# Kernel optimization log

Hardware: AMD Instinct MI355X
Metric: run time of the kernel (lower is better)

Reference implementation:

```python
import jax, jax.numpy as jnp
import numpy as np
from jax.ops import segment_sum, segment_max

N_NODES = 10000
N_EDGES = 160000
N_GRAPHS = 32
IN_DIM = 128
HID = 256
HEADS = 4


def setup_inputs() -> dict:
    key = jax.random.key(0)
    ks = jax.random.split(key, 12)
    x = jax.random.normal(ks[0], (N_NODES, IN_DIM), dtype=jnp.float32)
    edge_index = jax.random.randint(ks[1], (2, N_EDGES), 0, N_NODES, dtype=jnp.int64)
    batch = jnp.sort(jax.random.randint(ks[2], (N_NODES,), 0, N_GRAPHS, dtype=jnp.int64))
    s = 0.05
    params = {
        "W1": jax.random.normal(ks[3], (IN_DIM, HID), dtype=jnp.float32) * s,
        "b1": jnp.zeros((HID,), dtype=jnp.float32),
        "W2": jax.random.normal(ks[4], (HID, HID), dtype=jnp.float32) * s,
        "b2": jnp.zeros((HID,), dtype=jnp.float32),
        "Wg": jax.random.normal(ks[5], (HID, HEADS * HID), dtype=jnp.float32) * s,
        "att_src": jax.random.normal(ks[6], (HEADS, HID), dtype=jnp.float32) * s,
        "att_dst": jax.random.normal(ks[7], (HEADS, HID), dtype=jnp.float32) * s,
        "bg": jnp.zeros((HID,), dtype=jnp.float32),
        "W_heads": jax.random.normal(ks[8], (HID, 4), dtype=jnp.float32) * s,
        "b_heads": jnp.zeros((4,), dtype=jnp.float32),
    }
    return {"x": x, "edge_index": edge_index, "batch": batch, **params}


def _add_self_loops(edge_index, n):
    loop = jnp.arange(n, dtype=edge_index.dtype)
    src = jnp.concatenate([edge_index[0], loop])
    dst = jnp.concatenate([edge_index[1], loop])
    return src, dst


def _gcn_conv(x, W, b, src, dst, n):
    # PyG GCNConv: add self-loops, symmetric normalization D^-1/2 A D^-1/2
    h = x @ W                                   # [N, out]
    deg = segment_sum(jnp.ones_like(src, dtype=h.dtype), dst, num_segments=n)
    dinv = jax.lax.rsqrt(jnp.maximum(deg, 1e-12))
    coef = dinv[src] * dinv[dst]                # [E+N]
    out = segment_sum(h[src] * coef[:, None], dst, num_segments=n)
    return out + b


def _gat_conv(x, Wg, att_src, att_dst, bg, src, dst, n):
    # PyG GATConv(heads=4, concat=False): mean over heads, leaky_relu slope 0.2
    h = (x @ Wg).reshape(n, HEADS, HID)         # [N, H, C]
    a_src = jnp.einsum('nhc,hc->nh', h, att_src)
    a_dst = jnp.einsum('nhc,hc->nh', h, att_dst)
    e = jax.nn.leaky_relu(a_src[src] + a_dst[dst], 0.2)   # [E+N, H]
    m = segment_max(e, dst, num_segments=n)
    e = jnp.exp(e - m[dst])
    z = segment_sum(e, dst, num_segments=n)
    alpha = e / (z[dst] + 1e-16)                # softmax over edges into each dst
    out = segment_sum(h[src] * alpha[:, :, None], dst, num_segments=n)  # [N, H, C]
    return out.mean(axis=1) + bg


def reference(x, edge_index, batch, W1, b1, W2, b2, Wg, att_src, att_dst, bg, W_heads, b_heads):
    n = x.shape[0]
    src, dst = _add_self_loops(edge_index, n)
    h1 = jax.nn.relu(_gcn_conv(x, W1, b1, src, dst, n))
    h2 = jax.nn.relu(_gcn_conv(h1, W2, b2, src, dst, n))
    h3 = jax.nn.relu(_gat_conv(h2, Wg, att_src, att_dst, bg, src, dst, n))
    # global_mean_pool
    ones = jnp.ones((n,), dtype=h3.dtype)
    cnt = segment_sum(ones, batch, num_segments=N_GRAPHS)
    pooled = segment_sum(h3, batch, num_segments=N_GRAPHS) / jnp.maximum(cnt, 1.0)[:, None]
    # four scalar heads stacked: cols = [energy_absorption, elastic_modulus, ballistic_limit, penetration_resistance]
    return pooled @ W_heads + b_heads           # [G, 4]
```

## Files before the change

### kernel.cpp

```cpp
#include <hip/hip_runtime.h>
#include <cmath>

#define IN_DIM 128
#define HID 256
#define NHEADS 4
#define NGRAPHS 32

typedef unsigned short u16;
typedef __attribute__((ext_vector_type(8))) short bfrag8;
typedef __attribute__((ext_vector_type(4))) float f32x4;

__device__ __forceinline__ u16 f2bf(float x) {
  unsigned u = __float_as_uint(x);
  unsigned r = (u + 0x7fffu + ((u >> 16) & 1u)) >> 16;
  return (u16)r;
}
__device__ __forceinline__ float bf2f(u16 v) {
  return __uint_as_float(((unsigned)v) << 16);
}
__device__ __forceinline__ float lof(unsigned u) { return __uint_as_float(u << 16); }
__device__ __forceinline__ float hif(unsigned u) { return __uint_as_float(u & 0xffff0000u); }
__device__ __forceinline__ float lrelu02(float x) { return x > 0.f ? x : 0.2f * x; }

#define GACC(U, W)                                                   \
  acc[0] += (W) * lof((U).x); acc[1] += (W) * hif((U).x);            \
  acc[2] += (W) * lof((U).y); acc[3] += (W) * hif((U).y);            \
  acc[4] += (W) * lof((U).z); acc[5] += (W) * hif((U).z);            \
  acc[6] += (W) * lof((U).w); acc[7] += (W) * hif((U).w);

#define GACC2(U, W)                                                  \
  a0 += (W) * lof((U).x); a1 += (W) * hif((U).x);                    \
  a2 += (W) * lof((U).y); a3 += (W) * hif((U).y);

__global__ __launch_bounds__(256) void count_edges_k(const int* __restrict__ dst,
                                                     int* __restrict__ cnt, int E) {
  int i = blockIdx.x * 256 + threadIdx.x;
  if (i < E) atomicAdd(&cnt[dst[i]], 1);
}

__global__ __launch_bounds__(256) void fill_csr_k(const int* __restrict__ src,
                                                  const int* __restrict__ dst,
                                                  const int* __restrict__ row_ptr,
                                                  int* __restrict__ cursor,
                                                  int* __restrict__ csr_src, int E) {
  int i = blockIdx.x * 256 + threadIdx.x;
  if (i < E) {
    int d = dst[i];
    int p = atomicAdd(&cursor[d], 1);
    csr_src[row_ptr[d] + p] = src[i];
  }
}

__device__ void scan_dev(const int* __restrict__ cnt, int* __restrict__ row_ptr,
                         float* __restrict__ dinv, int n) {
  __shared__ int s_w[4];
  __shared__ int s_off[4];
  __shared__ int s_tot;
  int tid = threadIdx.x, wv = tid >> 6, lane = tid & 63;
  int carry = 0;
  int nch = (n + 255) >> 8;
  for (int c = 0; c < nch; c++) {
    int i = (c << 8) + tid;
    int v = (i < n) ? cnt[i] : 0;
    int incl = v;
    #pragma unroll
    for (int off = 1; off < 64; off <<= 1) {
      int t = __shfl_up(incl, off);
      if (lane >= off) incl += t;
    }
    if (lane == 63) s_w[wv] = incl;
    __syncthreads();
    if (tid == 0) {
      int a0 = s_w[0], a1 = s_w[1], a2 = s_w[2], a3 = s_w[3];
      s_off[0] = 0; s_off[1] = a0; s_off[2] = a0 + a1; s_off[3] = a0 + a1 + a2;
      s_tot = a0 + a1 + a2 + a3;
    }
    __syncthreads();
    int excl = incl - v + s_off[wv] + carry;
    if (i < n) {
      row_ptr[i] = excl;
      dinv[i] = rsqrtf((float)(v + 1));
    }
    carry += s_tot;
    __syncthreads();
  }
  if (tid == 0) row_ptr[n] = carry;
}

__device__ void pack_a_dev(const float* __restrict__ A, u16* __restrict__ Ap,
                           int K, int KT, int wid, int lane) {
  int fm = wid / KT, kt = wid - fm * KT;
  int m = fm * 16 + (lane & 15);
  int kb = kt * 32 + (lane >> 4) * 8;
  const float* src = A + (size_t)m * K + kb;
  float4 v0 = *(const float4*)src;
  float4 v1 = *(const float4*)(src + 4);
  float vv[8] = {v0.x, v0.y, v0.z, v0.w, v1.x, v1.y, v1.z, v1.w};
  u16 hi[8], lo[8];
  #pragma unroll
  for (int j = 0; j < 8; j++) {
    u16 h = f2bf(vv[j]);
    hi[j] = h;
    lo[j] = f2bf(vv[j] - bf2f(h));
  }
  u16* dstp = Ap + ((size_t)fm * KT + kt) * 1024 + lane * 8;
  *(ushort4*)(dstp)       = make_ushort4(hi[0], hi[1], hi[2], hi[3]);
  *(ushort4*)(dstp + 4)   = make_ushort4(hi[4], hi[5], hi[6], hi[7]);
  *(ushort4*)(dstp + 512) = make_ushort4(lo[0], lo[1], lo[2], lo[3]);
  *(ushort4*)(dstp + 516) = make_ushort4(lo[4], lo[5], lo[6], lo[7]);
}

__device__ void pack_b_dev(const float* __restrict__ B, u16* __restrict__ Bp,
                           int N, int KT, int wid, int lane) {
  int fn = wid / KT, kt = wid - fn * KT;
  int n = fn * 16 + (lane & 15);
  int kb = kt * 32 + (lane >> 4) * 8;
  float vv[8];
  #pragma unroll
  for (int j = 0; j < 8; j++) vv[j] = B[(size_t)(kb + j) * N + n];
  u16 hi[8], lo[8];
  #pragma unroll
  for (int j = 0; j < 8; j++) {
    u16 h = f2bf(vv[j]);
    hi[j] = h;
    lo[j] = f2bf(vv[j] - bf2f(h));
  }
  u16* dstp = Bp + ((size_t)fn * KT + kt) * 1024 + lane * 8;
  *(ushort4*)(dstp)       = make_ushort4(hi[0], hi[1], hi[2], hi[3]);
  *(ushort4*)(dstp + 4)   = make_ushort4(hi[4], hi[5], hi[6], hi[7]);
  *(ushort4*)(dstp + 512) = make_ushort4(lo[0], lo[1], lo[2], lo[3]);
  *(ushort4*)(dstp + 516) = make_ushort4(lo[4], lo[5], lo[6], lo[7]);
}

__global__ __launch_bounds__(256) void prep_k(const float* __restrict__ x,
                                              const float* __restrict__ W1,
                                              const float* __restrict__ W2,
                                              const float* __restrict__ Wg,
                                              const float* __restrict__ att_src,
                                              const float* __restrict__ att_dst,
                                              const int* __restrict__ cnt,
                                              int* __restrict__ row_ptr,
                                              float* __restrict__ dinv,
                                              u16* __restrict__ xp,
                                              u16* __restrict__ w1p,
                                              u16* __restrict__ w2p,
                                              u16* __restrict__ wgp,
                                              float* __restrict__ w_s,
                                              float* __restrict__ w_d,
                                              int NFM, int N) {
  __shared__ float red_s[4][NHEADS];
  __shared__ float red_d[4][NHEADS];
  int b = blockIdx.x;
  int tid = threadIdx.x;
  int lane = tid & 63;
  if (b == 0) {
    scan_dev(cnt, row_ptr, dinv, N);
    return;
  }
  b -= 1;
  int XB = NFM;
  if (b < XB) {
    int wid = b * 4 + (tid >> 6);
    if (wid < NFM * 4) pack_a_dev(x, xp, IN_DIM, 4, wid, lane);
  } else if (b < XB + 16) {
    pack_b_dev(W1, w1p, HID, 4, (b - XB) * 4 + (tid >> 6), lane);
  } else if (b < XB + 48) {
    pack_b_dev(W2, w2p, HID, 8, (b - XB - 16) * 4 + (tid >> 6), lane);
  } else if (b < XB + 176) {
    pack_b_dev(Wg, wgp, NHEADS * HID, 8, (b - XB - 48) * 4 + (tid >> 6), lane);
  } else {
    int k = b - (XB + 176);
    int c = tid, wvv = c >> 6, ln = c & 63;
    #pragma unroll
    for (int h = 0; h < NHEADS; h++) {
      float w = Wg[(size_t)k * (NHEADS * HID) + h * HID + c];
      float vs = w * att_src[h * HID + c];
      float vd = w * att_dst[h * HID + c];
      #pragma unroll
      for (int off = 32; off; off >>= 1) {
        vs += __shfl_xor(vs, off);
        vd += __shfl_xor(vd, off);
      }
      if (ln == 0) { red_s[wvv][h] = vs; red_d[wvv][h] = vd; }
    }
    __syncthreads();
    if (c < NHEADS)
      w_s[k * NHEADS + c] = red_s[0][c] + red_s[1][c] + red_s[2][c] + red_s[3][c];
    else if (c < 2 * NHEADS) {
      int h = c - NHEADS;
      w_d[k * NHEADS + h] = red_d[0][h] + red_d[1][h] + red_d[2][h] + red_d[3][h];
    }
  }
}

template <int KT, int LDC, bool ALO>
__global__ __launch_bounds__(256) void mfma_gemm_k(const u16* __restrict__ Ap,
                                                   const u16* __restrict__ Bp,
                                                   u16* __restrict__ Cb, int M) {
  int tid = threadIdx.x;
  int w = tid >> 6, lane = tid & 63;
  int wm = w >> 1, wn = w & 1;
  int fm0 = blockIdx.y * 4 + wm * 2;
  int fn0 = blockIdx.x * 4 + wn * 2;
  f32x4 acc[2][2] = {};
  #pragma unroll
  for (int kt = 0; kt < KT; kt++) {
    bfrag8 a_hi[2], a_lo[2], b_hi[2], b_lo[2];
    #pragma unroll
    for (int f = 0; f < 2; f++) {
      const u16* pa = Ap + ((size_t)(fm0 + f) * KT + kt) * 1024 + lane * 8;
      a_hi[f] = *(const bfrag8*)pa;
      if constexpr (ALO) a_lo[f] = *(const bfrag8*)(pa + 512);
      const u16* pb = Bp + ((size_t)(fn0 + f) * KT + kt) * 1024 + lane * 8;
      b_hi[f] = *(const bfrag8*)pb;
      b_lo[f] = *(const bfrag8*)(pb + 512);
    }
    #pragma unroll
    for (int f = 0; f < 2; f++) {
      #pragma unroll
      for (int g = 0; g < 2; g++) {
        acc[f][g] = __builtin_amdgcn_mfma_f32_16x16x32_bf16(a_hi[f], b_hi[g], acc[f][g], 0, 0, 0);
        acc[f][g] = __builtin_amdgcn_mfma_f32_16x16x32_bf16(a_hi[f], b_lo[g], acc[f][g], 0, 0, 0);
        if constexpr (ALO)
          acc[f][g] = __builtin_amdgcn_mfma_f32_16x16x32_bf16(a_lo[f], b_hi[g], acc[f][g], 0, 0, 0);
      }
    }
  }
  int r0 = (lane >> 4) * 4;
  int cl = lane & 15;
  #pragma unroll
  for (int f = 0; f < 2; f++) {
    #pragma unroll
    for (int g = 0; g < 2; g++) {
      int col = (fn0 + g) * 16 + cl;
      #pragma unroll
      for (int r = 0; r < 4; r++) {
        int row = (fm0 + f) * 16 + r0 + r;
        if (row < M) Cb[(size_t)row * LDC + col] = f2bf(acc[f][g][r]);
      }
    }
  }
}

template <bool LOGITS, bool PACK_LO>
__global__ __launch_bounds__(256) void gcn_agg_k(const u16* __restrict__ t,
                                                 const int* __restrict__ row_ptr,
                                                 const int* __restrict__ csr_src,
                                                 const float* __restrict__ dinv,
                                                 const float* __restrict__ bias,
                                                 u16* __restrict__ apack,
                                                 const float* __restrict__ w_s,
                                                 const float* __restrict__ w_d,
                                                 float4* __restrict__ a_src4,
                                                 float4* __restrict__ a_dst4, int N) {
  int wv = threadIdx.x >> 6, lane = threadIdx.x & 63;
  int i = blockIdx.x * 4 + wv;
  if (i >= N) return;
  float di = dinv[i];
  int c4 = lane * 4;
  int beg = row_ptr[i], end = row_ptr[i + 1];
  float a0, a1, a2, a3;
  {
    uint2 u = *(const uint2*)&t[(size_t)i * HID + c4];
    float w = di * di;
    a0 = w * lof(u.x); a1 = w * hif(u.x); a2 = w * lof(u.y); a3 = w * hif(u.y);
  }
  int e = beg;
  for (; e + 3 < end; e += 4) {
    int s0 = csr_src[e + 0], s1 = csr_src[e + 1];
    int s2 = csr_src[e + 2], s3 = csr_src[e + 3];
    float w0 = dinv[s0] * di, w1 = dinv[s1] * di;
    float w2 = dinv[s2] * di, w3 = dinv[s3] * di;
    uint2 u0 = *(const uint2*)&t[(size_t)s0 * HID + c4];
    uint2 u1 = *(const uint2*)&t[(size_t)s1 * HID + c4];
    uint2 u2 = *(const uint2*)&t[(size_t)s2 * HID + c4];
    uint2 u3 = *(const uint2*)&t[(size_t)s3 * HID + c4];
    GACC2(u0, w0); GACC2(u1, w1); GACC2(u2, w2); GACC2(u3, w3);
  }
  for (; e < end; e++) {
    int s = csr_src[e];
    float w = dinv[s] * di;
    uint2 u = *(const uint2*)&t[(size_t)s * HID + c4];
    GACC2(u, w);
  }
  float4 bv = *(const float4*)&bias[c4];
  float v0 = fmaxf(a0 + bv.x, 0.f), v1 = fmaxf(a1 + bv.y, 0.f);
  float v2 = fmaxf(a2 + bv.z, 0.f), v3 = fmaxf(a3 + bv.w, 0.f);
  {
    int fm = i >> 4, kt = c4 >> 5;
    int pl = (i & 15) + 16 * ((c4 >> 3) & 3);
    int j = c4 & 7;
    size_t base = ((size_t)fm * 8 + kt) * 1024 + pl * 8 + j;
    u16 h0 = f2bf(v0), h1 = f2bf(v1), h2 = f2bf(v2), h3 = f2bf(v3);
    *(ushort4*)&apack[base] = make_ushort4(h0, h1, h2, h3);
    if constexpr (PACK_LO)
      *(ushort4*)&apack[base + 512] =
          make_ushort4(f2bf(v0 - bf2f(h0)), f2bf(v1 - bf2f(h1)),
                       f2bf(v2 - bf2f(h2)), f2bf(v3 - bf2f(h3)));
  }
  if constexpr (LOGITS) {
    const float4* ws4 = (const float4*)w_s;
    const float4* wd4 = (const float4*)w_d;
    float4 s0 = ws4[c4 + 0], s1 = ws4[c4 + 1], s2 = ws4[c4 + 2], s3 = ws4[c4 + 3];
    float4 d0 = wd4[c4 + 0], d1 = wd4[c4 + 1], d2 = wd4[c4 + 2], d3 = wd4[c4 + 3];
    float ps0 = v0 * s0.x + v1 * s1.x + v2 * s2.x + v3 * s3.x;
    float ps1 = v0 * s0.y + v1 * s1.y + v2 * s2.y + v3 * s3.y;
    float ps2 = v0 * s0.z + v1 * s1.z + v2 * s2.z + v3 * s3.z;
    float ps3 = v0 * s0.w + v1 * s1.w + v2 * s2.w + v3 * s3.w;
    float pd0 = v0 * d0.x + v1 * d1.x + v2 * d2.x + v3 * d3.x;
    float pd1 = v0 * d0.y + v1 * d1.y + v2 * d2.y + v3 * d3.y;
    float pd2 = v0 * d0.z + v1 * d1.z + v2 * d2.z + v3 * d3.z;
    float pd3 = v0 * d0.w + v1 * d1.w + v2 * d2.w + v3 * d3.w;
    #pragma unroll
    for (int off = 32; off; off >>= 1) {
      ps0 += __shfl_xor(ps0, off); ps1 += __shfl_xor(ps1, off);
      ps2 += __shfl_xor(ps2, off); ps3 += __shfl_xor(ps3, off);
      pd0 += __shfl_xor(pd0, off); pd1 += __shfl_xor(pd1, off);
      pd2 += __shfl_xor(pd2, off); pd3 += __shfl_xor(pd3, off);
    }
    if (lane == 0) {
      a_src4[i] = make_float4(ps0, ps1, ps2, ps3);
      a_dst4[i] = make_float4(pd0, pd1, pd2, pd3);
    }
  }
}

__global__ __launch_bounds__(256) void gat_agg_k(const u16* __restrict__ hgT,
                                                 const int* __restrict__ row_ptr,
                                                 const int* __restrict__ csr_src,
                                                 const float4* __restrict__ a_src4,
                                                 const float4* __restrict__ a_dst4,
                                                 const float* __restrict__ bg,
                                                 float* __restrict__ out, int N) {
  __shared__ int s_src[4][64];
  __shared__ float s_al[4][2][64];
  __shared__ float s_comb[2][32][9];
  int wv = threadIdx.x >> 6, lane = threadIdx.x & 63;
  int nodeSlot = wv >> 1, half = wv & 1;
  int i = blockIdx.x * 2 + nodeSlot;
  if (i >= N) { __syncthreads(); return; }
  int beg = row_ptr[i], end = row_ptr[i + 1];
  int deg = end - beg;
  float4 ad = a_dst4[i];
  int hsel = lane >> 5;
  const u16* rowbase = hgT + half * 512 + lane * 8;
  float acc[8];
  #pragma unroll
  for (int j = 0; j < 8; j++) acc[j] = 0.f;

  if (deg <= 63) {
    int s = (lane < deg) ? csr_src[beg + lane] : i;
    bool valid = (lane <= deg);
    float4 as = a_src4[s];
    float l0 = valid ? lrelu02(as.x + ad.x) : -INFINITY;
    float l1 = valid ? lrelu02(as.y + ad.y) : -INFINITY;
    float l2 = valid ? lrelu02(as.z + ad.z) : -INFINITY;
    float l3 = valid ? lrelu02(as.w + ad.w) : -INFINITY;
    float m0 = l0, m1 = l1, m2 = l2, m3 = l3;
    #pragma unroll
    for (int off = 32; off; off >>= 1) {
      m0 = fmaxf(m0, __shfl_xor(m0, off)); m1 = fmaxf(m1, __shfl_xor(m1, off));
      m2 = fmaxf(m2, __shfl_xor(m2, off)); m3 = fmaxf(m3, __shfl_xor(m3, off));
    }
    float e0 = valid ? expf(l0 - m0) : 0.f;
    float e1 = valid ? expf(l1 - m1) : 0.f;
    float e2 = valid ? expf(l2 - m2) : 0.f;
    float e3 = valid ? expf(l3 - m3) : 0.f;
    float z0 = e0, z1 = e1, z2 = e2, z3 = e3;
    #pragma unroll
    for (int off = 32; off; off >>= 1) {
      z0 += __shfl_xor(z0, off); z1 += __shfl_xor(z1, off);
      z2 += __shfl_xor(z2, off); z3 += __shfl_xor(z3, off);
    }
    s_src[wv][lane] = s;
    if (half == 0) {
      s_al[wv][0][lane] = e0 / (z0 + 1e-16f);
      s_al[wv][1][lane] = e1 / (z1 + 1e-16f);
    } else {
      s_al[wv][0][lane] = e2 / (z2 + 1e-16f);
      s_al[wv][1][lane] = e3 / (z3 + 1e-16f);
    }
    int nk = deg + 1;
    int e = 0;
    for (; e + 3 < nk; e += 4) {
      int sa = s_src[wv][e + 0], sb = s_src[wv][e + 1];
      int sc = s_src[wv][e + 2], sd = s_src[wv][e + 3];
      float wa = s_al[wv][hsel][e + 0], wb = s_al[wv][hsel][e + 1];
      float wc = s_al[wv][hsel][e + 2], wd = s_al[wv][hsel][e + 3];
      uint4 ua = *(const uint4*)(rowbase + (size_t)sa * 1024);
      uint4 ub = *(const uint4*)(rowbase + (size_t)sb * 1024);
      uint4 uc = *(const uint4*)(rowbase + (size_t)sc * 1024);
      uint4 ud = *(const uint4*)(rowbase + (size_t)sd * 1024);
      GACC(ua, wa); GACC(ub, wb); GACC(uc, wc); GACC(ud, wd);
    }
    for (; e < nk; e++) {
      int sa = s_src[wv][e];
      float wa = s_al[wv][hsel][e];
      uint4 ua = *(const uint4*)(rowbase + (size_t)sa * 1024);
      GACC(ua, wa);
    }
  } else {
    float4 asi = a_src4[i];
    float ls0 = lrelu02(asi.x + ad.x), ls1 = lrelu02(asi.y + ad.y);
    float ls2 = lrelu02(asi.z + ad.z), ls3 = lrelu02(asi.w + ad.w);
    float m0 = ls0, m1 = ls1, m2 = ls2, m3 = ls3;
    for (int e = beg + lane; e < end; e += 64) {
      float4 as = a_src4[csr_src[e]];
      m0 = fmaxf(m0, lrelu02(as.x + ad.x)); m1 = fmaxf(m1, lrelu02(as.y + ad.y));
      m2 = fmaxf(m2, lrelu02(as.z + ad.z)); m3 = fmaxf(m3, lrelu02(as.w + ad.w));
    }
    #pragma unroll
    for (int off = 32; off; off >>= 1) {
      m0 = fmaxf(m0, __shfl_xor(m0, off)); m1 = fmaxf(m1, __shfl_xor(m1, off));
      m2 = fmaxf(m2, __shfl_xor(m2, off)); m3 = fmaxf(m3, __shfl_xor(m3, off));
    }
    float z0 = (lane == 0) ? expf(ls0 - m0) : 0.f;
    float z1 = (lane == 0) ? expf(ls1 - m1) : 0.f;
    float z2 = (lane == 0) ? expf(ls2 - m2) : 0.f;
    float z3 = (lane == 0) ? expf(ls3 - m3) : 0.f;
    for (int e = beg + lane; e < end; e += 64) {
      float4 as = a_src4[csr_src[e]];
      z0 += expf(lrelu02(as.x + ad.x) - m0); z1 += expf(lrelu02(as.y + ad.y) - m1);
      z2 += expf(lrelu02(as.z + ad.z) - m2); z3 += expf(lrelu02(as.w + ad.w) - m3);
    }
    #pragma unroll
    for (int off = 32; off; off >>= 1) {
      z0 += __shfl_xor(z0, off); z1 += __shfl_xor(z1, off);
      z2 += __shfl_xor(z2, off); z3 += __shfl_xor(z3, off);
    }
    float iz0 = 1.f / (z0 + 1e-16f), iz1 = 1.f / (z1 + 1e-16f);
    float iz2 = 1.f / (z2 + 1e-16f), iz3 = 1.f / (z3 + 1e-16f);
    {
      float w0 = expf(ls0 - m0) * iz0, w1 = expf(ls1 - m1) * iz1;
      float w2 = expf(ls2 - m2) * iz2, w3 = expf(ls3 - m3) * iz3;
      float aw = (half == 0) ? (hsel == 0 ? w0 : w1) : (hsel == 0 ? w2 : w3);
      uint4 u = *(const uint4*)(rowbase + (size_t)i * 1024);
      GACC(u, aw);
    }
    for (int base = beg; base < end; base += 64) {
      int mc = min(64, end - base);
      if (lane < mc) {
        int s = csr_src[base + lane];
        float4 as = a_src4[s];
        s_src[wv][lane] = s;
        if (half == 0) {
          s_al[wv][0][lane] = expf(lrelu02(as.x + ad.x) - m0) * iz0;
          s_al[wv][1][lane] = expf(lrelu02(as.y + ad.y) - m1) * iz1;
        } else {
          s_al[wv][0][lane] = expf(lrelu02(as.z + ad.z) - m2) * iz2;
          s_al[wv][1][lane] = expf(lrelu02(as.w + ad.w) - m3) * iz3;
        }
      }
      for (int e = 0; e < mc; e++) {
        int sa = s_src[wv][e];
        float wa = s_al[wv][hsel][e];
        uint4 ua = *(const uint4*)(rowbase + (size_t)sa * 1024);
        GACC(ua, wa);
      }
    }
  }
  #pragma unroll
  for (int j = 0; j < 8; j++) acc[j] += __shfl_xor(acc[j], 32);
  if (half == 1 && lane < 32) {
    #pragma unroll
    for (int j = 0; j < 8; j++) s_comb[nodeSlot][lane][j] = acc[j];
  }
  __syncthreads();
  if (half == 0 && lane < 32) {
    int cb = lane * 8;
    float o[8];
    #pragma unroll
    for (int j = 0; j < 8; j++)
      o[j] = fmaxf((acc[j] + s_comb[nodeSlot][lane][j]) * 0.25f + bg[cb + j], 0.f);
    float* op = out + (size_t)i * HID + cb;
    *(float4*)(op + 0) = make_float4(o[0], o[1], o[2], o[3]);
    *(float4*)(op + 4) = make_float4(o[4], o[5], o[6], o[7]);
  }
}

__global__ __launch_bounds__(256) void pool_head_k(const float* __restrict__ h3,
                                                   const int* __restrict__ batch,
                                                   const float* __restrict__ W_heads,
                                                   const float* __restrict__ b_heads,
                                                   float* __restrict__ out, int N) {
  int g = blockIdx.x >> 3;
  int part = blockIdx.x & 7;
  int c = threadIdx.x;
  __shared__ int s_bounds[2];
  if (c < 2) {
    int target = g + c;
    int lo = 0, hi = N;
    while (lo < hi) {
      int mid = (lo + hi) >> 1;
      if (batch[mid] < target) lo = mid + 1; else hi = mid;
    }
    s_bounds[c] = lo;
  }
  __syncthreads();
  int i0 = s_bounds[0], i1 = s_bounds[1];
  float acc0 = 0.f, acc1 = 0.f;
  int i = i0 + part;
  for (; i + 8 < i1; i += 16) {
    acc0 += h3[(size_t)i * HID + c];
    acc1 += h3[(size_t)(i + 8) * HID + c];
  }
  if (i < i1) acc0 += h3[(size_t)i * HID + c];
  float acc = acc0 + acc1;
  float invc = 1.f / fmaxf((float)(i1 - i0), 1.f);
  float4 wh = *(const float4*)&W_heads[c * 4];
  float p0 = acc * wh.x, p1 = acc * wh.y, p2 = acc * wh.z, p3 = acc * wh.w;
  int lane = c & 63, wv = c >> 6;
  #pragma unroll
  for (int off = 32; off; off >>= 1) {
    p0 += __shfl_xor(p0, off); p1 += __shfl_xor(p1, off);
    p2 += __shfl_xor(p2, off); p3 += __shfl_xor(p3, off);
  }
  __shared__ float s_red[4][4];
  if (lane == 0) { s_red[wv][0] = p0; s_red[wv][1] = p1; s_red[wv][2] = p2; s_red[wv][3] = p3; }
  __syncthreads();
  if (c < 4) {
    float r = s_red[0][c] + s_red[1][c] + s_red[2][c] + s_red[3][c];
    atomicAdd(&out[g * 4 + c], r * invc + b_heads[c] * 0.125f);
  }
}

extern "C" void kernel_launch(void* const* d_in, const int* in_sizes, int n_in,
                              void* d_out, int out_size, void* d_ws, size_t ws_size,
                              hipStream_t stream) {
  const float* x = (const float*)d_in[0];
  const int* ei = (const int*)d_in[1];
  const int* batch = (const int*)d_in[2];
  const float* W1 = (const float*)d_in[3];
  const float* b1 = (const float*)d_in[4];
  const float* W2 = (const float*)d_in[5];
  const float* b2 = (const float*)d_in[6];
  const float* Wg = (const float*)d_in[7];
  const float* att_src = (const float*)d_in[8];
  const float* att_dst = (const float*)d_in[9];
  const float* bg = (const float*)d_in[10];
  const float* W_heads = (const float*)d_in[11];
  const float* b_heads = (const float*)d_in[12];
  float* out = (float*)d_out;

  const int N = in_sizes[0] / IN_DIM;
  const int E = in_sizes[1] / 2;
  const int* src = ei;
  const int* dst = ei + E;

  const int NFM = N / 16;
  const int NFMP = ((N + 63) / 64) * 4;

  char* ws = (char*)d_ws;
  size_t off = 0;
  auto take = [&](size_t bytes) -> char* {
    char* p = ws + off;
    off = (off + bytes + 255) & ~(size_t)255;
    return p;
  };
  int* cnt      = (int*)take((size_t)N * 4);
  int* cursor   = (int*)take((size_t)N * 4);
  size_t zero_span = off;
  int* row_ptr  = (int*)take((size_t)(N + 1) * 4);
  int* csr_src  = (int*)take((size_t)E * 4);
  float* dinv   = (float*)take((size_t)N * 4);
  float4* a_src4 = (float4*)take((size_t)N * 16);
  float4* a_dst4 = (float4*)take((size_t)N * 16);
  float* w_s    = (float*)take((size_t)HID * NHEADS * 4);
  float* w_d    = (float*)take((size_t)HID * NHEADS * 4);
  u16*   tb     = (u16*)take((size_t)N * HID * 2);
  float* h3     = (float*)take((size_t)N * HID * 4);
  u16*   hgT    = (u16*)take((size_t)N * NHEADS * HID * 2);
  u16*   xp     = (u16*)take((size_t)NFMP * 4 * 1024 * 2);
  u16*   h1p    = (u16*)take((size_t)NFMP * 8 * 1024 * 2);
  u16*   h2p    = (u16*)take((size_t)NFMP * 8 * 1024 * 2);
  u16*   w1p    = (u16*)take((size_t)16 * 4 * 1024 * 2);
  u16*   w2p    = (u16*)take((size_t)16 * 8 * 1024 * 2);
  u16*   wgp    = (u16*)take((size_t)64 * 8 * 1024 * 2);

  hipMemsetAsync(cnt, 0, zero_span, stream);
  hipMemsetAsync(out, 0, (size_t)out_size * 4, stream);

  int eb = (E + 255) / 256;
  count_edges_k<<<eb, 256, 0, stream>>>(dst, cnt, E);
  prep_k<<<1 + NFM + 176 + 256, 256, 0, stream>>>(x, W1, W2, Wg, att_src, att_dst,
                                                  cnt, row_ptr, dinv,
                                                  xp, w1p, w2p, wgp, w_s, w_d, NFM, N);
  fill_csr_k<<<eb, 256, 0, stream>>>(src, dst, row_ptr, cursor, csr_src, E);

  int mg64 = (N + 63) / 64;
  int ng4 = (N + 3) / 4;
  int ng2 = (N + 1) / 2;
  mfma_gemm_k<4, HID, true><<<dim3(4, mg64), 256, 0, stream>>>(xp, w1p, tb, N);
  gcn_agg_k<false, true><<<ng4, 256, 0, stream>>>(tb, row_ptr, csr_src, dinv, b1,
                                                  h1p, nullptr, nullptr, nullptr, nullptr, N);
  mfma_gemm_k<8, HID, true><<<dim3(4, mg64), 256, 0, stream>>>(h1p, w2p, tb, N);
  gcn_agg_k<true, false><<<ng4, 256, 0, stream>>>(tb, row_ptr, csr_src, dinv, b2,
                                                  h2p, w_s, w_d, a_src4, a_dst4, N);
  mfma_gemm_k<8, NHEADS * HID, false><<<dim3(16, mg64), 256, 0, stream>>>(h2p, wgp, hgT, N);
  gat_agg_k<<<ng2, 256, 0, stream>>>(hgT, row_ptr, csr_src, a_src4, a_dst4, bg, h3, N);
  pool_head_k<<<NGRAPHS * 8, 256, 0, stream>>>(h3, batch, W_heads, b_heads, out, N);
}
```

Measured before the change: 197.9 us.

## Fuse mean-pool and regression heads into GAT aggregation; drop A-lo split precision

The global mean pool and the four-column head projection move into the GAT aggregation epilogue. Each node projects its ReLU output onto W_heads, scales by a precomputed inverse graph count, and atomically adds into the output. The output is initialised with the bias in prep_k, which also computes the per-graph counts by binary search. This removes the h3 write and read and the separate pool kernel. Separately, the low-order bf16 part of the A operand is no longer packed or multiplied, which cuts one MFMA in three for the first two GEMMs at some cost in accuracy. The trade-off is many more atomics per graph output and float atomic nondeterminism.

```diff
diff --git a/kernel.cpp b/kernel.cpp
--- a/kernel.cpp
+++ b/kernel.cpp
@@ -87,6 +87,7 @@
   if (tid == 0) row_ptr[n] = carry;
 }
 
+template <bool LO>
 __device__ void pack_a_dev(const float* __restrict__ A, u16* __restrict__ Ap,
                            int K, int KT, int wid, int lane) {
   int fm = wid / KT, kt = wid - fm * KT;
@@ -96,18 +97,19 @@
   float4 v0 = *(const float4*)src;
   float4 v1 = *(const float4*)(src + 4);
   float vv[8] = {v0.x, v0.y, v0.z, v0.w, v1.x, v1.y, v1.z, v1.w};
-  u16 hi[8], lo[8];
-  #pragma unroll
-  for (int j = 0; j < 8; j++) {
-    u16 h = f2bf(vv[j]);
-    hi[j] = h;
-    lo[j] = f2bf(vv[j] - bf2f(h));
-  }
+  u16 hi[8];
+  #pragma unroll
+  for (int j = 0; j < 8; j++) hi[j] = f2bf(vv[j]);
   u16* dstp = Ap + ((size_t)fm * KT + kt) * 1024 + lane * 8;
-  *(ushort4*)(dstp)       = make_ushort4(hi[0], hi[1], hi[2], hi[3]);
-  *(ushort4*)(dstp + 4)   = make_ushort4(hi[4], hi[5], hi[6], hi[7]);
-  *(ushort4*)(dstp + 512) = make_ushort4(lo[0], lo[1], lo[2], lo[3]);
-  *(ushort4*)(dstp + 516) = make_ushort4(lo[4], lo[5], lo[6], lo[7]);
+  *(ushort4*)(dstp)     = make_ushort4(hi[0], hi[1], hi[2], hi[3]);
+  *(ushort4*)(dstp + 4) = make_ushort4(hi[4], hi[5], hi[6], hi[7]);
+  if constexpr (LO) {
+    u16 lo[8];
+    #pragma unroll
+    for (int j = 0; j < 8; j++) lo[j] = f2bf(vv[j] - bf2f(hi[j]));
+    *(ushort4*)(dstp + 512) = make_ushort4(lo[0], lo[1], lo[2], lo[3]);
+    *(ushort4*)(dstp + 516) = make_ushort4(lo[4], lo[5], lo[6], lo[7]);
+  }
 }
 
 __device__ void pack_b_dev(const float* __restrict__ B, u16* __restrict__ Bp,
@@ -147,6 +149,10 @@
                                               u16* __restrict__ wgp,
                                               float* __restrict__ w_s,
                                               float* __restrict__ w_d,
+                                              const int* __restrict__ batch,
+                                              float* __restrict__ ginv,
+                                              const float* __restrict__ b_heads,
+                                              float* __restrict__ outp,
                                               int NFM, int N) {
   __shared__ float red_s[4][NHEADS];
   __shared__ float red_d[4][NHEADS];
@@ -161,14 +167,14 @@
   int XB = NFM;
   if (b < XB) {
     int wid = b * 4 + (tid >> 6);
-    if (wid < NFM * 4) pack_a_dev(x, xp, IN_DIM, 4, wid, lane);
+    if (wid < NFM * 4) pack_a_dev<false>(x, xp, IN_DIM, 4, wid, lane);
   } else if (b < XB + 16) {
     pack_b_dev(W1, w1p, HID, 4, (b - XB) * 4 + (tid >> 6), lane);
   } else if (b < XB + 48) {
     pack_b_dev(W2, w2p, HID, 8, (b - XB - 16) * 4 + (tid >> 6), lane);
   } else if (b < XB + 176) {
     pack_b_dev(Wg, wgp, NHEADS * HID, 8, (b - XB - 48) * 4 + (tid >> 6), lane);
-  } else {
+  } else if (b < XB + 432) {
     int k = b - (XB + 176);
     int c = tid, wvv = c >> 6, ln = c & 63;
     #pragma unroll
@@ -190,10 +196,25 @@
       int h = c - NHEADS;
       w_d[k * NHEADS + h] = red_d[0][h] + red_d[1][h] + red_d[2][h] + red_d[3][h];
     }
-  }
-}
-
-template <int KT, int LDC, bool ALO>
+  } else {
+    __shared__ int s_b[NGRAPHS + 1];
+    if (tid <= NGRAPHS) {
+      int target = tid;
+      int lo = 0, hi = N;
+      while (lo < hi) {
+        int mid = (lo + hi) >> 1;
+        if (batch[mid] < target) lo = mid + 1; else hi = mid;
+      }
+      s_b[tid] = lo;
+    }
+    __syncthreads();
+    if (tid < NGRAPHS)
+      ginv[tid] = 1.f / fmaxf((float)(s_b[tid + 1] - s_b[tid]), 1.f);
+    if (tid < NGRAPHS * 4) outp[tid] = b_heads[tid & 3];
+  }
+}
+
+template <int KT, int LDC>
 __global__ __launch_bounds__(256) void mfma_gemm_k(const u16* __restrict__ Ap,
                                                    const u16* __restrict__ Bp,
                                                    u16* __restrict__ Cb, int M) {
@@ -205,12 +226,11 @@
   f32x4 acc[2][2] = {};
   #pragma unroll
   for (int kt = 0; kt < KT; kt++) {
-    bfrag8 a_hi[2], a_lo[2], b_hi[2], b_lo[2];
+    bfrag8 a_hi[2], b_hi[2], b_lo[2];
     #pragma unroll
     for (int f = 0; f < 2; f++) {
       const u16* pa = Ap + ((size_t)(fm0 + f) * KT + kt) * 1024 + lane * 8;
       a_hi[f] = *(const bfrag8*)pa;
-      if constexpr (ALO) a_lo[f] = *(const bfrag8*)(pa + 512);
       const u16* pb = Bp + ((size_t)(fn0 + f) * KT + kt) * 1024 + lane * 8;
       b_hi[f] = *(const bfrag8*)pb;
       b_lo[f] = *(const bfrag8*)(pb + 512);
@@ -221,8 +241,6 @@
       for (int g = 0; g < 2; g++) {
         acc[f][g] = __builtin_amdgcn_mfma_f32_16x16x32_bf16(a_hi[f], b_hi[g], acc[f][g], 0, 0, 0);
         acc[f][g] = __builtin_amdgcn_mfma_f32_16x16x32_bf16(a_hi[f], b_lo[g], acc[f][g], 0, 0, 0);
-        if constexpr (ALO)
-          acc[f][g] = __builtin_amdgcn_mfma_f32_16x16x32_bf16(a_lo[f], b_hi[g], acc[f][g], 0, 0, 0);
       }
     }
   }
@@ -242,7 +260,7 @@
   }
 }
 
-template <bool LOGITS, bool PACK_LO>
+template <bool LOGITS>
 __global__ __launch_bounds__(256) void gcn_agg_k(const u16* __restrict__ t,
                                                  const int* __restrict__ row_ptr,
                                                  const int* __restrict__ csr_src,
@@ -291,12 +309,7 @@
     int pl = (i & 15) + 16 * ((c4 >> 3) & 3);
     int j = c4 & 7;
     size_t base = ((size_t)fm * 8 + kt) * 1024 + pl * 8 + j;
-    u16 h0 = f2bf(v0), h1 = f2bf(v1), h2 = f2bf(v2), h3 = f2bf(v3);
-    *(ushort4*)&apack[base] = make_ushort4(h0, h1, h2, h3);
-    if constexpr (PACK_LO)
-      *(ushort4*)&apack[base + 512] =
-          make_ushort4(f2bf(v0 - bf2f(h0)), f2bf(v1 - bf2f(h1)),
-                       f2bf(v2 - bf2f(h2)), f2bf(v3 - bf2f(h3)));
+    *(ushort4*)&apack[base] = make_ushort4(f2bf(v0), f2bf(v1), f2bf(v2), f2bf(v3));
   }
   if constexpr (LOGITS) {
     const float4* ws4 = (const float4*)w_s;
@@ -331,7 +344,10 @@
                                                  const float4* __restrict__ a_src4,
                                                  const float4* __restrict__ a_dst4,
                                                  const float* __restrict__ bg,
-                                                 float* __restrict__ out, int N) {
+                                                 const float* __restrict__ W_heads,
+                                                 const float* __restrict__ ginv,
+                                                 const int* __restrict__ batch,
+                                                 float* __restrict__ outp, int N) {
   __shared__ int s_src[4][64];
   __shared__ float s_al[4][2][64];
   __shared__ float s_comb[2][32][9];
@@ -468,59 +484,26 @@
   __syncthreads();
   if (half == 0 && lane < 32) {
     int cb = lane * 8;
-    float o[8];
-    #pragma unroll
-    for (int j = 0; j < 8; j++)
-      o[j] = fmaxf((acc[j] + s_comb[nodeSlot][lane][j]) * 0.25f + bg[cb + j], 0.f);
-    float* op = out + (size_t)i * HID + cb;
-    *(float4*)(op + 0) = make_float4(o[0], o[1], o[2], o[3]);
-    *(float4*)(op + 4) = make_float4(o[4], o[5], o[6], o[7]);
-  }
-}
-
-__global__ __launch_bounds__(256) void pool_head_k(const float* __restrict__ h3,
-                                                   const int* __restrict__ batch,
-                                                   const float* __restrict__ W_heads,
-                                                   const float* __restrict__ b_heads,
-                                                   float* __restrict__ out, int N) {
-  int g = blockIdx.x >> 3;
-  int part = blockIdx.x & 7;
-  int c = threadIdx.x;
-  __shared__ int s_bounds[2];
-  if (c < 2) {
-    int target = g + c;
-    int lo = 0, hi = N;
-    while (lo < hi) {
-      int mid = (lo + hi) >> 1;
-      if (batch[mid] < target) lo = mid + 1; else hi = mid;
-    }
-    s_bounds[c] = lo;
-  }
-  __syncthreads();
-  int i0 = s_bounds[0], i1 = s_bounds[1];
-  float acc0 = 0.f, acc1 = 0.f;
-  int i = i0 + part;
-  for (; i + 8 < i1; i += 16) {
-    acc0 += h3[(size_t)i * HID + c];
-    acc1 += h3[(size_t)(i + 8) * HID + c];
-  }
-  if (i < i1) acc0 += h3[(size_t)i * HID + c];
-  float acc = acc0 + acc1;
-  float invc = 1.f / fmaxf((float)(i1 - i0), 1.f);
-  float4 wh = *(const float4*)&W_heads[c * 4];
-  float p0 = acc * wh.x, p1 = acc * wh.y, p2 = acc * wh.z, p3 = acc * wh.w;
-  int lane = c & 63, wv = c >> 6;
-  #pragma unroll
-  for (int off = 32; off; off >>= 1) {
-    p0 += __shfl_xor(p0, off); p1 += __shfl_xor(p1, off);
-    p2 += __shfl_xor(p2, off); p3 += __shfl_xor(p3, off);
-  }
-  __shared__ float s_red[4][4];
-  if (lane == 0) { s_red[wv][0] = p0; s_red[wv][1] = p1; s_red[wv][2] = p2; s_red[wv][3] = p3; }
-  __syncthreads();
-  if (c < 4) {
-    float r = s_red[0][c] + s_red[1][c] + s_red[2][c] + s_red[3][c];
-    atomicAdd(&out[g * 4 + c], r * invc + b_heads[c] * 0.125f);
+    float p0 = 0.f, p1 = 0.f, p2 = 0.f, p3 = 0.f;
+    #pragma unroll
+    for (int j = 0; j < 8; j++) {
+      float o = fmaxf((acc[j] + s_comb[nodeSlot][lane][j]) * 0.25f + bg[cb + j], 0.f);
+      float4 wh = *(const float4*)&W_heads[(cb + j) * 4];
+      p0 += o * wh.x; p1 += o * wh.y; p2 += o * wh.z; p3 += o * wh.w;
+    }
+    #pragma unroll
+    for (int off = 16; off; off >>= 1) {
+      p0 += __shfl_xor(p0, off); p1 += __shfl_xor(p1, off);
+      p2 += __shfl_xor(p2, off); p3 += __shfl_xor(p3, off);
+    }
+    if (lane == 0) {
+      int g = batch[i];
+      float iv = ginv[g];
+      atomicAdd(&outp[g * 4 + 0], p0 * iv);
+      atomicAdd(&outp[g * 4 + 1], p1 * iv);
+      atomicAdd(&outp[g * 4 + 2], p2 * iv);
+      atomicAdd(&outp[g * 4 + 3], p3 * iv);
+    }
   }
 }
 
@@ -567,8 +550,8 @@
   float4* a_dst4 = (float4*)take((size_t)N * 16);
   float* w_s    = (float*)take((size_t)HID * NHEADS * 4);
   float* w_d    = (float*)take((size_t)HID * NHEADS * 4);
+  float* ginv   = (float*)take((size_t)NGRAPHS * 4);
   u16*   tb     = (u16*)take((size_t)N * HID * 2);
-  float* h3     = (float*)take((size_t)N * HID * 4);
   u16*   hgT    = (u16*)take((size_t)N * NHEADS * HID * 2);
   u16*   xp     = (u16*)take((size_t)NFMP * 4 * 1024 * 2);
   u16*   h1p    = (u16*)take((size_t)NFMP * 8 * 1024 * 2);
@@ -578,25 +561,25 @@
   u16*   wgp    = (u16*)take((size_t)64 * 8 * 1024 * 2);
 
   hipMemsetAsync(cnt, 0, zero_span, stream);
-  hipMemsetAsync(out, 0, (size_t)out_size * 4, stream);
 
   int eb = (E + 255) / 256;
   count_edges_k<<<eb, 256, 0, stream>>>(dst, cnt, E);
-  prep_k<<<1 + NFM + 176 + 256, 256, 0, stream>>>(x, W1, W2, Wg, att_src, att_dst,
-                                                  cnt, row_ptr, dinv,
-                                                  xp, w1p, w2p, wgp, w_s, w_d, NFM, N);
+  prep_k<<<1 + NFM + 432 + 1, 256, 0, stream>>>(x, W1, W2, Wg, att_src, att_dst,
+                                                cnt, row_ptr, dinv,
+                                                xp, w1p, w2p, wgp, w_s, w_d,
+                                                batch, ginv, b_heads, out, NFM, N);
   fill_csr_k<<<eb, 256, 0, stream>>>(src, dst, row_ptr, cursor, csr_src, E);
 
   int mg64 = (N + 63) / 64;
   int ng4 = (N + 3) / 4;
   int ng2 = (N + 1) / 2;
-  mfma_gemm_k<4, HID, true><<<dim3(4, mg64), 256, 0, stream>>>(xp, w1p, tb, N);
-  gcn_agg_k<false, true><<<ng4, 256, 0, stream>>>(tb, row_ptr, csr_src, dinv, b1,
-                                                  h1p, nullptr, nullptr, nullptr, nullptr, N);
-  mfma_gemm_k<8, HID, true><<<dim3(4, mg64), 256, 0, stream>>>(h1p, w2p, tb, N);
-  gcn_agg_k<true, false><<<ng4, 256, 0, stream>>>(tb, row_ptr, csr_src, dinv, b2,
-                                                  h2p, w_s, w_d, a_src4, a_dst4, N);
-  mfma_gemm_k<8, NHEADS * HID, false><<<dim3(16, mg64), 256, 0, stream>>>(h2p, wgp, hgT, N);
-  gat_agg_k<<<ng2, 256, 0, stream>>>(hgT, row_ptr, csr_src, a_src4, a_dst4, bg, h3, N);
-  pool_head_k<<<NGRAPHS * 8, 256, 0, stream>>>(h3, batch, W_heads, b_heads, out, N);
-}
+  mfma_gemm_k<4, HID><<<dim3(4, mg64), 256, 0, stream>>>(xp, w1p, tb, N);
+  gcn_agg_k<false><<<ng4, 256, 0, stream>>>(tb, row_ptr, csr_src, dinv, b1,
+                                            h1p, nullptr, nullptr, nullptr, nullptr, N);
+  mfma_gemm_k<8, HID><<<dim3(4, mg64), 256, 0, stream>>>(h1p, w2p, tb, N);
+  gcn_agg_k<true><<<ng4, 256, 0, stream>>>(tb, row_ptr, csr_src, dinv, b2,
+                                           h2p, w_s, w_d, a_src4, a_dst4, N);
+  mfma_gemm_k<8, NHEADS * HID><<<dim3(16, mg64), 256, 0, stream>>>(h2p, wgp, hgT, N);
+  gat_agg_k<<<ng2, 256, 0, stream>>>(hgT, row_ptr, csr_src, a_src4, a_dst4, bg,
+                                     W_heads, ginv, batch, out, N);
+}
```

Result: slower. 382.3 us (+93.2%).
